# Kernel tuning notes

Hardware: AMD Instinct MI355X
Metric: run time of the kernel (lower is better)

## Reference

```python
import jax, jax.numpy as jnp
import numpy as np

B, N, F, S, OUT = 8, 12000, 128, 16, 128

def setup_inputs() -> dict:
    key = jax.random.key(0)
    k1, k2, k3, k4 = jax.random.split(key, 4)
    x = jax.random.normal(k1, (B, N, F), dtype=jnp.float32)
    # Linear(in_c*spiral_size, out_c): weight [out, in], bias [out]
    bound = 1.0 / np.sqrt(F * S)
    W = jax.random.uniform(k2, (OUT, F * S), dtype=jnp.float32, minval=-bound, maxval=bound)
    b = jax.random.uniform(k3, (OUT,), dtype=jnp.float32, minval=-bound, maxval=bound)
    spiral_adj = jax.random.randint(k4, (1, N, S), 0, N, dtype=jnp.int32)
    zero_padding = jnp.ones((1, N, 1), dtype=jnp.float32)
    return {"x": x, "W": W, "b": b, "spiral_adj": spiral_adj, "zero_padding": zero_padding}

def reference(x, W, b, spiral_adj, zero_padding):
    # x: [B, N, F]; spiral_adj: [1, N, S] vertex indices shared across batch
    idx = spiral_adj[0]                         # [N, S]
    spirals = x[:, idx, :]                      # [B, N, S, F] gather along vertex dim
    bsz, npts, s, f = spirals.shape
    spirals = spirals.reshape(bsz, npts, s * f)  # [B, N, S*F]
    out = jnp.einsum('bnk,ok->bno', spirals, W) + b  # [B, N, OUT]
    out = jax.nn.relu(out)
    return out * zero_padding
```

## Files before the change

### kernel.cpp

```cpp
#include <hip/hip_runtime.h>

#define BATCH 8
#define NPTS  12000
#define FDIM  128
#define SDIM  16
#define ODIM  128
#define KDIM  (SDIM * FDIM)
#define MTOT  (BATCH * NPTS)

#define BM 128
#define BK 64

#define NTILES 94
#define XELEMS (BATCH * NPTS * FDIM)
#define WELEMS (ODIM * KDIM)
#define XBYTES ((size_t)XELEMS * 2)
#define WBYTES ((size_t)WELEMS * 2)
#define XN4    (XELEMS / 4)
#define WN4    (WELEMS / 4)

typedef __bf16 bf16x4 __attribute__((ext_vector_type(4)));
typedef __bf16 bf16x8 __attribute__((ext_vector_type(8)));
typedef float  f32x4  __attribute__((ext_vector_type(4)));
typedef float  f32x8  __attribute__((ext_vector_type(8)));

#define AS1(p) ((const __attribute__((address_space(1))) void*)(p))
#define AS3(p) ((__attribute__((address_space(3))) void*)(p))

__global__ __launch_bounds__(256)
void cvt_f32_bf16(const float* __restrict__ x, const float* __restrict__ W,
                  __bf16* __restrict__ xb, __bf16* __restrict__ Wb) {
    int i = blockIdx.x * blockDim.x + threadIdx.x;
    const int stride = gridDim.x * blockDim.x;
    for (; i < XN4 + WN4; i += stride) {
        const float* src; __bf16* dst; int j;
        if (i < XN4) { src = x; dst = xb; j = i; }
        else         { src = W; dst = Wb; j = i - XN4; }
        const float4 v = reinterpret_cast<const float4*>(src)[j];
        bf16x4 h;
        h[0] = (__bf16)v.x; h[1] = (__bf16)v.y;
        h[2] = (__bf16)v.z; h[3] = (__bf16)v.w;
        reinterpret_cast<bf16x4*>(dst)[j] = h;
    }
}

__global__ __launch_bounds__(256, 4)
void spiral_gemm_bf16(const __bf16* __restrict__ xb,
                      const __bf16* __restrict__ Wb,
                      const float*  __restrict__ bias,
                      const int*    __restrict__ idx,
                      const float*  __restrict__ zp,
                      float*        __restrict__ out)
{
    __shared__ __bf16 As[BM * BK];
    __shared__ __bf16 Ws[ODIM * BK];

    const int tid   = threadIdx.x;
    const int wave  = tid >> 6;
    const int lane  = tid & 63;
    const int batch = blockIdx.x & 7;
    const int n0    = (blockIdx.x >> 3) * BM;

    const int lrow8 = lane >> 3;
    const int clog  = (lane & 7) ^ lrow8;

    const __bf16* xbase = xb + (size_t)batch * (NPTS * FDIM);

    int nn[4], gcur[4], gnext[4];
#pragma unroll
    for (int p = 0; p < 4; ++p) {
        const int r = (p * 4 + wave) * 8 + lrow8;
        int n = n0 + r;
        nn[p]   = n < NPTS ? n : NPTS - 1;
        gcur[p] = idx[nn[p] * SDIM + 0];
    }

    f32x4 acc[4][4];
#pragma unroll
    for (int i = 0; i < 4; ++i)
#pragma unroll
        for (int j = 0; j < 4; ++j)
            acc[i][j] = f32x4{0.f, 0.f, 0.f, 0.f};

    const int wm   = (wave >> 1) * 64;
    const int wn   = (wave & 1) * 64;
    const int lrow = lane & 15;
    const int quad = lane >> 4;

    for (int kt = 0; kt < KDIM / BK; ++kt) {
        const int f0 = (kt & 1) * BK;
        __syncthreads();
#pragma unroll
        for (int p = 0; p < 4; ++p) {
            const int r0 = (p * 4 + wave) * 8;
            const __bf16* ga = xbase + (size_t)gcur[p] * FDIM + f0 + clog * 8;
            __builtin_amdgcn_global_load_lds(AS1(ga), AS3(&As[r0 * BK]), 16, 0, 0);
            const __bf16* gw = Wb + (size_t)(r0 + lrow8) * KDIM + kt * BK + clog * 8;
            __builtin_amdgcn_global_load_lds(AS1(gw), AS3(&Ws[r0 * BK]), 16, 0, 0);
        }
        if ((kt & 1) && kt < KDIM / BK - 1) {
            const int snext = (kt >> 1) + 1;
#pragma unroll
            for (int p = 0; p < 4; ++p) gnext[p] = idx[nn[p] * SDIM + snext];
        }
        __syncthreads();
#pragma unroll
        for (int kk = 0; kk < 2; ++kk) {
            const int ph = (kk * 4 + quad) ^ (lrow & 7);
            bf16x8 a[4], b[4];
#pragma unroll
            for (int i = 0; i < 4; ++i)
                a[i] = *reinterpret_cast<const bf16x8*>(
                    &As[(wm + i * 16 + lrow) * BK + ph * 8]);
#pragma unroll
            for (int j = 0; j < 4; ++j)
                b[j] = *reinterpret_cast<const bf16x8*>(
                    &Ws[(wn + j * 16 + lrow) * BK + ph * 8]);
#pragma unroll
            for (int i = 0; i < 4; ++i)
#pragma unroll
                for (int j = 0; j < 4; ++j)
                    acc[i][j] = __builtin_amdgcn_mfma_f32_16x16x32_bf16(
                        a[i], b[j], acc[i][j], 0, 0, 0);
        }
        if (kt & 1) {
#pragma unroll
            for (int p = 0; p < 4; ++p) gcur[p] = gnext[p];
        }
    }

#pragma unroll
    for (int i = 0; i < 4; ++i) {
#pragma unroll
        for (int r = 0; r < 4; ++r) {
            const int row = wm + i * 16 + quad * 4 + r;
            const int n   = n0 + row;
            if (n < NPTS) {
                const float z = zp[n];
                float* orow   = out + ((size_t)batch * NPTS + n) * ODIM;
#pragma unroll
                for (int j = 0; j < 4; ++j) {
                    const int col = wn + j * 16 + lrow;
                    float v = acc[i][j][r] + bias[col];
                    v = fmaxf(v, 0.f);
                    orow[col] = v * z;
                }
            }
        }
    }
}

#define LDA 72
__global__ __launch_bounds__(256, 2)
void spiral_gemm_fp32(const float* __restrict__ x, const float* __restrict__ W,
                      const float* __restrict__ bias, const int* __restrict__ idx,
                      const float* __restrict__ zp, float* __restrict__ out)
{
    __shared__ __bf16 Asf[BM * LDA];
    __shared__ __bf16 Wsf[ODIM * LDA];
    const int tid = threadIdx.x, wave = tid >> 6, lane = tid & 63;
    const int m0 = blockIdx.x * BM;
    const int srow = tid >> 3, schunk = tid & 7;
    int a_n[4]; const float* a_xb[4];
#pragma unroll
    for (int p = 0; p < 4; ++p) {
        int m = m0 + srow + p * 32, bb = m / NPTS;
        a_n[p] = m - bb * NPTS; a_xb[p] = x + (size_t)bb * (NPTS * FDIM);
    }
    f32x4 acc[4][4];
#pragma unroll
    for (int i = 0; i < 4; ++i)
#pragma unroll
        for (int j = 0; j < 4; ++j) acc[i][j] = f32x4{0.f,0.f,0.f,0.f};
    const int wm = (wave >> 1) * 64, wn = (wave & 1) * 64;
    const int lrow = lane & 15, quad = lane >> 4;
    for (int kt = 0; kt < KDIM / BK; ++kt) {
        const int s = kt >> 1, f0 = (kt & 1) * BK;
        __syncthreads();
#pragma unroll
        for (int p = 0; p < 4; ++p) {
            const int r = srow + p * 32;
            const int g = idx[a_n[p] * SDIM + s];
            const f32x8 v = *reinterpret_cast<const f32x8*>(
                a_xb[p] + (size_t)g * FDIM + f0 + schunk * 8);
            bf16x8 h;
#pragma unroll
            for (int e = 0; e < 8; ++e) h[e] = (__bf16)v[e];
            *reinterpret_cast<bf16x8*>(&Asf[r * LDA + schunk * 8]) = h;
            const f32x8 w = *reinterpret_cast<const f32x8*>(
                W + (size_t)r * KDIM + kt * BK + schunk * 8);
            bf16x8 hw;
#pragma unroll
            for (int e = 0; e < 8; ++e) hw[e] = (__bf16)w[e];
            *reinterpret_cast<bf16x8*>(&Wsf[r * LDA + schunk * 8]) = hw;
        }
        __syncthreads();
#pragma unroll
        for (int kk = 0; kk < 2; ++kk) {
            const int koff = kk * 32 + quad * 8;
            bf16x8 a[4], b[4];
#pragma unroll
            for (int i = 0; i < 4; ++i)
                a[i] = *reinterpret_cast<const bf16x8*>(&Asf[(wm + i*16 + lrow)*LDA + koff]);
#pragma unroll
            for (int j = 0; j < 4; ++j)
                b[j] = *reinterpret_cast<const bf16x8*>(&Wsf[(wn + j*16 + lrow)*LDA + koff]);
#pragma unroll
            for (int i = 0; i < 4; ++i)
#pragma unroll
                for (int j = 0; j < 4; ++j)
                    acc[i][j] = __builtin_amdgcn_mfma_f32_16x16x32_bf16(a[i], b[j], acc[i][j], 0,0,0);
        }
    }
#pragma unroll
    for (int i = 0; i < 4; ++i)
#pragma unroll
        for (int r = 0; r < 4; ++r) {
            const int row = wm + i * 16 + quad * 4 + r;
            const int m = m0 + row, bb = m / NPTS, nnn = m - bb * NPTS;
            const float z = zp[nnn];
            float* orow = out + (size_t)m * ODIM;
#pragma unroll
            for (int j = 0; j < 4; ++j) {
                const int col = wn + j * 16 + lrow;
                float v = acc[i][j][r] + bias[col];
                orow[col] = fmaxf(v, 0.f) * z;
            }
        }
}

extern "C" void kernel_launch(void* const* d_in, const int* in_sizes, int n_in,
                              void* d_out, int out_size, void* d_ws, size_t ws_size,
                              hipStream_t stream) {
    const float* x    = (const float*)d_in[0];
    const float* W    = (const float*)d_in[1];
    const float* bias = (const float*)d_in[2];
    const int*   idx  = (const int*)d_in[3];
    const float* zp   = (const float*)d_in[4];
    float*       out  = (float*)d_out;

    if (ws_size >= XBYTES + WBYTES) {
        __bf16* xb = (__bf16*)d_ws;
        __bf16* Wb = (__bf16*)((char*)d_ws + XBYTES);
        cvt_f32_bf16<<<dim3(1024), dim3(256), 0, stream>>>(x, W, xb, Wb);
        spiral_gemm_bf16<<<dim3(BATCH * NTILES), dim3(256), 0, stream>>>(
            xb, Wb, bias, idx, zp, out);
    } else {
        spiral_gemm_fp32<<<dim3(MTOT / BM), dim3(256), 0, stream>>>(
            x, W, bias, idx, zp, out);
    }
}
```

Baseline: 165.2 us.

## Double-buffer LDS tiles with async prefetch and stage spiral indices in shared memory

Splits the A and W LDS tiles into two buffers so the next K-tile's global-to-LDS loads are issued before the current tile is computed. Partial vmcnt waits and explicit barriers replace the old double syncthreads per iteration. The block's spiral indices are also preloaded into shared memory once, instead of re-reading them from global memory every other step. This doubles LDS use and lowers the launch-bounds occupancy hint from 4 to 2 blocks, and the hand-written waitcnt logic depends on the compiler not reordering memory operations.

```diff
diff --git a/kernel.cpp b/kernel.cpp
--- a/kernel.cpp
+++ b/kernel.cpp
@@ -44,7 +44,7 @@
     }
 }
 
-__global__ __launch_bounds__(256, 4)
+__global__ __launch_bounds__(256, 2)
 void spiral_gemm_bf16(const __bf16* __restrict__ xb,
                       const __bf16* __restrict__ Wb,
                       const float*  __restrict__ bias,
@@ -52,8 +52,9 @@
                       const float*  __restrict__ zp,
                       float*        __restrict__ out)
 {
-    __shared__ __bf16 As[BM * BK];
-    __shared__ __bf16 Ws[ODIM * BK];
+    __shared__ __bf16 As[2][BM * BK];
+    __shared__ __bf16 Ws[2][ODIM * BK];
+    __shared__ int    idxS[BM * SDIM];
 
     const int tid   = threadIdx.x;
     const int wave  = tid >> 6;
@@ -66,14 +67,36 @@
 
     const __bf16* xbase = xb + (size_t)batch * (NPTS * FDIM);
 
-    int nn[4], gcur[4], gnext[4];
-#pragma unroll
-    for (int p = 0; p < 4; ++p) {
-        const int r = (p * 4 + wave) * 8 + lrow8;
-        int n = n0 + r;
-        nn[p]   = n < NPTS ? n : NPTS - 1;
-        gcur[p] = idx[nn[p] * SDIM + 0];
-    }
+    {
+        const int row  = tid >> 1, half = tid & 1;
+        const int n    = n0 + row;
+        const int nrow = n < NPTS ? n : NPTS - 1;
+        const int4* s4 = reinterpret_cast<const int4*>(idx + nrow * SDIM + half * 8);
+        int4* d4       = reinterpret_cast<int4*>(&idxS[row * SDIM + half * 8]);
+        d4[0] = s4[0];
+        d4[1] = s4[1];
+    }
+    __syncthreads();
+
+    int rrow[4];
+#pragma unroll
+    for (int p = 0; p < 4; ++p) rrow[p] = (p * 4 + wave) * 8 + lrow8;
+
+    int gCur[4], gNext[4];
+#pragma unroll
+    for (int p = 0; p < 4; ++p) gCur[p] = idxS[rrow[p] * SDIM + 0];
+
+    auto issue = [&](int buf, int kt, const int* g) {
+        const int f0 = (kt & 1) * BK;
+#pragma unroll
+        for (int p = 0; p < 4; ++p) {
+            const int r0 = (p * 4 + wave) * 8;
+            const __bf16* ga = xbase + (size_t)g[p] * FDIM + f0 + clog * 8;
+            __builtin_amdgcn_global_load_lds(AS1(ga), AS3(&As[buf][r0 * BK]), 16, 0, 0);
+            const __bf16* gw = Wb + (size_t)(r0 + lrow8) * KDIM + kt * BK + clog * 8;
+            __builtin_amdgcn_global_load_lds(AS1(gw), AS3(&Ws[buf][r0 * BK]), 16, 0, 0);
+        }
+    };
 
     f32x4 acc[4][4];
 #pragma unroll
@@ -87,23 +110,7 @@
     const int lrow = lane & 15;
     const int quad = lane >> 4;
 
-    for (int kt = 0; kt < KDIM / BK; ++kt) {
-        const int f0 = (kt & 1) * BK;
-        __syncthreads();
-#pragma unroll
-        for (int p = 0; p < 4; ++p) {
-            const int r0 = (p * 4 + wave) * 8;
-            const __bf16* ga = xbase + (size_t)gcur[p] * FDIM + f0 + clog * 8;
-            __builtin_amdgcn_global_load_lds(AS1(ga), AS3(&As[r0 * BK]), 16, 0, 0);
-            const __bf16* gw = Wb + (size_t)(r0 + lrow8) * KDIM + kt * BK + clog * 8;
-            __builtin_amdgcn_global_load_lds(AS1(gw), AS3(&Ws[r0 * BK]), 16, 0, 0);
-        }
-        if ((kt & 1) && kt < KDIM / BK - 1) {
-            const int snext = (kt >> 1) + 1;
-#pragma unroll
-            for (int p = 0; p < 4; ++p) gnext[p] = idx[nn[p] * SDIM + snext];
-        }
-        __syncthreads();
+    auto compute = [&](int buf) {
 #pragma unroll
         for (int kk = 0; kk < 2; ++kk) {
             const int ph = (kk * 4 + quad) ^ (lrow & 7);
@@ -111,11 +118,11 @@
 #pragma unroll
             for (int i = 0; i < 4; ++i)
                 a[i] = *reinterpret_cast<const bf16x8*>(
-                    &As[(wm + i * 16 + lrow) * BK + ph * 8]);
+                    &As[buf][(wm + i * 16 + lrow) * BK + ph * 8]);
 #pragma unroll
             for (int j = 0; j < 4; ++j)
                 b[j] = *reinterpret_cast<const bf16x8*>(
-                    &Ws[(wn + j * 16 + lrow) * BK + ph * 8]);
+                    &Ws[buf][(wn + j * 16 + lrow) * BK + ph * 8]);
 #pragma unroll
             for (int i = 0; i < 4; ++i)
 #pragma unroll
@@ -123,10 +130,33 @@
                     acc[i][j] = __builtin_amdgcn_mfma_f32_16x16x32_bf16(
                         a[i], b[j], acc[i][j], 0, 0, 0);
         }
-        if (kt & 1) {
-#pragma unroll
-            for (int p = 0; p < 4; ++p) gcur[p] = gnext[p];
-        }
+    };
+
+    issue(0, 0, gCur);
+
+    for (int t = 0; t < 16; ++t) {
+        issue(1, 2 * t + 1, gCur);
+        asm volatile("s_waitcnt vmcnt(8)" ::: "memory");
+        asm volatile("s_barrier" ::: "memory");
+        if (t < 15) {
+#pragma unroll
+            for (int p = 0; p < 4; ++p)
+                gNext[p] = idxS[rrow[p] * SDIM + t + 1];
+        }
+        compute(0);
+        asm volatile("s_barrier" ::: "memory");
+
+        if (t < 15) {
+            issue(0, 2 * t + 2, gNext);
+            asm volatile("s_waitcnt vmcnt(8)" ::: "memory");
+        } else {
+            asm volatile("s_waitcnt vmcnt(0)" ::: "memory");
+        }
+        asm volatile("s_barrier" ::: "memory");
+        compute(1);
+        asm volatile("s_barrier" ::: "memory");
+#pragma unroll
+        for (int p = 0; p < 4; ++p) gCur[p] = gNext[p];
     }
 
 #pragma unroll
```

After: 163.6 us. Within noise of the previous version (-0.9%).
